# Kernel tuning notes

Hardware: AMD Instinct MI355X
Metric: run time of the kernel (lower is better)

Reference implementation:

```python
import jax, jax.numpy as jnp
import numpy as np
from jax import lax

WBITS = 2
ABITS = 2
STRIDES = (1, 1)
PADDING = 'SAME'


def _ste_quantize(x, k):
    # round(x * n) / n with straight-through gradient (identity)
    n = float(2 ** k - 1)
    q = jnp.round(x * n) / n
    return x + lax.stop_gradient(q - x)


def _quantize_weight(w, k):
    # DoReFa-style weight quantization: tanh, normalize to [0,1], quantize, map to [-1,1]
    t = jnp.tanh(w)
    t = t / jnp.max(jnp.abs(t)) * 0.5 + 0.5
    return 2.0 * _ste_quantize(t, k) - 1.0


def _quantize_act(x, k):
    return _ste_quantize(jnp.clip(x, 0.0, 1.0), k)


def setup_inputs() -> dict:
    key = jax.random.key(0)
    kx, kw = jax.random.split(key)
    x = jax.random.uniform(kx, (32, 56, 56, 256), dtype=jnp.float32)  # NHWC
    w = jax.random.normal(kw, (3, 3, 256, 256), dtype=jnp.float32) * 0.2  # HWIO
    # match init normalization: unit L2 norm per output channel over (h,w,cin)
    w = w / jnp.sqrt(1e-7 + jnp.sum(w * w, axis=(0, 1, 2), keepdims=True))
    return {'x': x, 'w': w}


def reference(x, w) -> jnp.ndarray:
    wq = _quantize_weight(w, WBITS)        # low-bit weights in [-1, 1]
    xq = _quantize_act(x, ABITS)           # low-bit activations in [0, 1]
    out = lax.conv_general_dilated(
        xq, wq,
        window_strides=STRIDES,
        padding=PADDING,
        dimension_numbers=('NHWC', 'HWIO', 'NHWC'),
    )
    return out
```

## Files before the change

kernel.cpp:

```cpp
#include <hip/hip_runtime.h>
#include <stdint.h>

#define GLOBAL_AS __attribute__((address_space(1)))
#define LDS_AS    __attribute__((address_space(3)))

typedef int   v4i  __attribute__((ext_vector_type(4)));
typedef int   v8i  __attribute__((ext_vector_type(8)));
typedef float v16f __attribute__((ext_vector_type(16)));

__device__ __forceinline__ void gload_lds16(const void* g, void* l) {
    __builtin_amdgcn_global_load_lds((GLOBAL_AS uint32_t*)g, (LDS_AS uint32_t*)l, 16, 0, 0);
}


__global__ void k_xq_wmax(const float* __restrict__ x, const float* __restrict__ w,
                          int8_t* __restrict__ xqp, unsigned* __restrict__ maxbits) {
    const int bid = blockIdx.x;
    if (bid < 48) {
        int t = bid * 256 + threadIdx.x;
        const float4* w4 = (const float4*)w;
        float m = 0.f;
        for (int i = t; i < 147456; i += 12288) {
            float4 v = w4[i];
            m = fmaxf(m, fmaxf(fmaxf(fabsf(tanhf(v.x)), fabsf(tanhf(v.y))),
                               fmaxf(fabsf(tanhf(v.z)), fabsf(tanhf(v.w)))));
        }
#pragma unroll
        for (int off = 32; off > 0; off >>= 1)
            m = fmaxf(m, __shfl_xor(m, off, 64));
        if ((threadIdx.x & 63) == 0) atomicMax(maxbits, __float_as_uint(m));
        return;
    }
    int t = (bid - 48) * 256 + threadIdx.x;
    int g  = t & 7;
    int p  = t >> 3;
    int xp = p % 58;
    int q  = p / 58;
    int yp = q % 58;
    int n  = q / 58;
    int4 r;
    if (yp == 0 || yp == 57 || xp == 0 || xp == 57) {
        r = make_int4(0, 0, 0, 0);
    } else {
        const float4* px = (const float4*)(x + (((long)((n * 56 + (yp - 1)) * 56 + (xp - 1))) << 8) + g * 32);
        int wds[4];
#pragma unroll
        for (int jj = 0; jj < 4; ++jj) {
            float4 v0 = px[jj * 2];
            float4 v1 = px[jj * 2 + 1];
            int q0 = (int)rintf(fminf(fmaxf(v0.x, 0.f), 1.f) * 3.f);
            int q1 = (int)rintf(fminf(fmaxf(v0.y, 0.f), 1.f) * 3.f);
            int q2 = (int)rintf(fminf(fmaxf(v0.z, 0.f), 1.f) * 3.f);
            int q3 = (int)rintf(fminf(fmaxf(v0.w, 0.f), 1.f) * 3.f);
            int q4 = (int)rintf(fminf(fmaxf(v1.x, 0.f), 1.f) * 3.f);
            int q5 = (int)rintf(fminf(fmaxf(v1.y, 0.f), 1.f) * 3.f);
            int q6 = (int)rintf(fminf(fmaxf(v1.z, 0.f), 1.f) * 3.f);
            int q7 = (int)rintf(fminf(fmaxf(v1.w, 0.f), 1.f) * 3.f);
            wds[jj] = ((0x5420 >> (q0 << 2)) & 0xF)        | (((0x5420 >> (q1 << 2)) & 0xF) << 4)
                    | (((0x5420 >> (q2 << 2)) & 0xF) << 8) | (((0x5420 >> (q3 << 2)) & 0xF) << 12)
                    | (((0x5420 >> (q4 << 2)) & 0xF) << 16)| (((0x5420 >> (q5 << 2)) & 0xF) << 20)
                    | (((0x5420 >> (q6 << 2)) & 0xF) << 24)| (((0x5420 >> (q7 << 2)) & 0xF) << 28);
        }
        r = make_int4(wds[0], wds[1], wds[2], wds[3]);
    }
    *(int4*)(xqp + ((long)t << 4)) = r;
}

__global__ void k_wq(const float* __restrict__ w, const unsigned* __restrict__ maxbits,
                     int8_t* __restrict__ wqt) {
    int t = blockIdx.x * 256 + threadIdx.x;
    int co = t & 255;
    int kblk = t >> 8;
    float inv = 0.5f / __uint_as_float(*maxbits);
    uint8_t b[16];
#pragma unroll
    for (int j = 0; j < 16; ++j) {
        float t0 = tanhf(w[(long)(kblk * 32 + 2 * j) * 256 + co]);
        float t1 = tanhf(w[(long)(kblk * 32 + 2 * j + 1) * 256 + co]);
        int q0 = (int)rintf((t0 * inv + 0.5f) * 3.0f);
        int q1 = (int)rintf((t1 * inv + 0.5f) * 3.0f);
        b[j] = (uint8_t)(((0x52AD >> (q0 << 2)) & 0xF) | (((0x52AD >> (q1 << 2)) & 0xF) << 4));
    }
    *(int4*)(wqt + (long)co * 1152 + kblk * 16) = *(int4*)b;
}

#define BM 128
#define BN 128

__global__ __launch_bounds__(256) void k_conv(const int8_t* __restrict__ xqp,
                                              const int8_t* __restrict__ wqt,
                                              float* __restrict__ out) {
    __shared__ int8_t sA[2][BM * 128];
    __shared__ int8_t sB[2][BN * 128];

    const int tid    = threadIdx.x;
    const int wv     = tid >> 6;
    const int lane   = tid & 63;
    const int orig   = blockIdx.x;
    const int work   = (orig & 7) * 196 + (orig >> 3);
    const int coBase = (work & 1) * BN;
    const int mBase  = (work >> 1) * BM;

    const int lr = lane >> 3;
    const int lp = lane & 7;
    const int8_t* aB[4];
    const int8_t* bB[4];
#pragma unroll
    for (int j = 0; j < 4; ++j) {
        int r = wv * 8 + j * 32 + lr;
        int g = lp ^ (r & 7);
        int m = mBase + r;
        int n = m / 3136;
        int rem = m - n * 3136;
        int y = rem / 56;
        int x = rem - y * 56;
        aB[j] = xqp + (((long)((n * 58 + y) * 58 + x)) << 7) + g * 16;
        bB[j] = wqt + (long)(coBase + r) * 1152 + g * 16;
    }

    v16f acc[2][2];
#pragma unroll
    for (int a = 0; a < 2; ++a)
#pragma unroll
        for (int b = 0; b < 2; ++b)
#pragma unroll
            for (int r = 0; r < 16; ++r) acc[a][b][r] = 0.f;

    const int wm  = (wv & 1) * 64;
    const int wn  = (wv >> 1) * 64;
    const int l31 = lane & 31;
    const int hi  = lane >> 5;

    const int rA0 = (wm + l31) * 128;       const int axr0 = ((wm + l31) & 7) << 4;
    const int rA1 = (wm + 32 + l31) * 128;  const int axr1 = ((wm + 32 + l31) & 7) << 4;
    const int rB0 = (wn + l31) * 128;       const int bxr0 = ((wn + l31) & 7) << 4;
    const int rB1 = (wn + 32 + l31) * 128;  const int bxr1 = ((wn + 32 + l31) & 7) << 4;

    auto issue = [&](int it, int b) {
        int ky  = it / 3;
        int kx  = it - ky * 3;
        int aOff = (ky * 58 + kx) << 7;
        int bOff = it << 7;
#pragma unroll
        for (int j = 0; j < 4; ++j) {
            gload_lds16(aB[j] + aOff, &sA[b][(wv * 8 + j * 32) * 128]);
            gload_lds16(bB[j] + bOff, &sB[b][(wv * 8 + j * 32) * 128]);
        }
    };

    const int SC = 0x7F7F7F7F;

    auto compute = [&](int b) {
        const int8_t* pA = sA[b];
        const int8_t* pB = sB[b];
        __builtin_amdgcn_s_setprio(1);
#pragma unroll
        for (int kk = 0; kk < 4; ++kk) {
            const int kc = (kk * 2 + hi) << 4;
            v4i a0 = *(const v4i*)(pA + rA0 + (kc ^ axr0));
            v4i a1 = *(const v4i*)(pA + rA1 + (kc ^ axr1));
            v4i b0 = *(const v4i*)(pB + rB0 + (kc ^ bxr0));
            v4i b1 = *(const v4i*)(pB + rB1 + (kc ^ bxr1));
            v8i A0 = {a0[0], a0[1], a0[2], a0[3], 0, 0, 0, 0};
            v8i A1 = {a1[0], a1[1], a1[2], a1[3], 0, 0, 0, 0};
            v8i B0 = {b0[0], b0[1], b0[2], b0[3], 0, 0, 0, 0};
            v8i B1 = {b1[0], b1[1], b1[2], b1[3], 0, 0, 0, 0};
            acc[0][0] = __builtin_amdgcn_mfma_scale_f32_32x32x64_f8f6f4(A0, B0, acc[0][0], 4, 4, 0, SC, 0, SC);
            acc[0][1] = __builtin_amdgcn_mfma_scale_f32_32x32x64_f8f6f4(A0, B1, acc[0][1], 4, 4, 0, SC, 0, SC);
            acc[1][0] = __builtin_amdgcn_mfma_scale_f32_32x32x64_f8f6f4(A1, B0, acc[1][0], 4, 4, 0, SC, 0, SC);
            acc[1][1] = __builtin_amdgcn_mfma_scale_f32_32x32x64_f8f6f4(A1, B1, acc[1][1], 4, 4, 0, SC, 0, SC);
        }
        __builtin_amdgcn_s_setprio(0);
    };

    issue(0, 0);
#pragma unroll 2
    for (int it = 0; it < 8; ++it) {
        issue(it + 1, (it + 1) & 1);
        asm volatile("s_waitcnt vmcnt(8)" ::: "memory");
        __builtin_amdgcn_s_barrier();
        asm volatile("" ::: "memory");
        compute(it & 1);
        asm volatile("" ::: "memory");
        __builtin_amdgcn_s_barrier();
        asm volatile("" ::: "memory");
    }
    asm volatile("s_waitcnt vmcnt(0)" ::: "memory");
    __builtin_amdgcn_s_barrier();
    asm volatile("" ::: "memory");
    compute(0);

    const float s = 1.0f / 9.0f;
#pragma unroll
    for (int mt = 0; mt < 2; ++mt) {
#pragma unroll
        for (int nt = 0; nt < 2; ++nt) {
            const int ocol = coBase + wn + nt * 32 + l31;
#pragma unroll
            for (int reg = 0; reg < 16; ++reg) {
                const int row = (reg & 3) + 8 * (reg >> 2) + 4 * hi;
                const long orow = mBase + wm + mt * 32 + row;
                out[orow * 256 + ocol] = acc[mt][nt][reg] * s;
            }
        }
    }
}

extern "C" void kernel_launch(void* const* d_in, const int* in_sizes, int n_in,
                              void* d_out, int out_size, void* d_ws, size_t ws_size,
                              hipStream_t stream) {
    const float* x = (const float*)d_in[0];
    const float* w = (const float*)d_in[1];
    float* out = (float*)d_out;

    unsigned* maxbits = (unsigned*)d_ws;
    int8_t* wqt = (int8_t*)d_ws + 4096;
    int8_t* xqp = (int8_t*)d_ws + 4096 + 294912;

    hipMemsetAsync(maxbits, 0, 4, stream);
    k_xq_wmax<<<48 + 3364, 256, 0, stream>>>(x, w, xqp, maxbits);
    k_wq<<<72, 256, 0, stream>>>(w, maxbits, wqt);
    k_conv<<<1568, 256, 0, stream>>>(xqp, wqt, out);
}
```

Before: 229.7 us.

## Stage halo pixel tile in LDS once and stream weights into registers

Each block now loads a single 256-pixel halo tile of padded, quantized activations into LDS once. All nine 3x3 taps are served from that tile by shifting the pixel offset, instead of reloading a 128-row A tile per tap. Weights are read directly from global memory into double-buffered registers, which removes the LDS B buffers and the per-iteration barriers. Tiles now follow image boundaries (25 tiles of 128 pixels per image), so some rows are computed and then masked at the store. Register pressure also rises from holding the B fragments.

```diff
diff --git a/kernel.cpp b/kernel.cpp
--- a/kernel.cpp
+++ b/kernel.cpp
@@ -84,113 +84,106 @@
     *(int4*)(wqt + (long)co * 1152 + kblk * 16) = *(int4*)b;
 }
 
-#define BM 128
-#define BN 128
-
-__global__ __launch_bounds__(256) void k_conv(const int8_t* __restrict__ xqp,
-                                              const int8_t* __restrict__ wqt,
-                                              float* __restrict__ out) {
-    __shared__ int8_t sA[2][BM * 128];
-    __shared__ int8_t sB[2][BN * 128];
-
-    const int tid    = threadIdx.x;
-    const int wv     = tid >> 6;
-    const int lane   = tid & 63;
-    const int orig   = blockIdx.x;
-    const int work   = (orig & 7) * 196 + (orig >> 3);
-    const int coBase = (work & 1) * BN;
-    const int mBase  = (work >> 1) * BM;
-
-    const int lr = lane >> 3;
-    const int lp = lane & 7;
-    const int8_t* aB[4];
-    const int8_t* bB[4];
-#pragma unroll
-    for (int j = 0; j < 4; ++j) {
-        int r = wv * 8 + j * 32 + lr;
-        int g = lp ^ (r & 7);
-        int m = mBase + r;
-        int n = m / 3136;
-        int rem = m - n * 3136;
-        int y = rem / 56;
-        int x = rem - y * 56;
-        aB[j] = xqp + (((long)((n * 58 + y) * 58 + x)) << 7) + g * 16;
-        bB[j] = wqt + (long)(coBase + r) * 1152 + g * 16;
-    }
-
-    v16f acc[2][2];
-#pragma unroll
-    for (int a = 0; a < 2; ++a)
-#pragma unroll
-        for (int b = 0; b < 2; ++b)
-#pragma unroll
-            for (int r = 0; r < 16; ++r) acc[a][b][r] = 0.f;
+__global__ __launch_bounds__(256, 3) void k_conv(const int8_t* __restrict__ xqp,
+                                                 const int8_t* __restrict__ wqt,
+                                                 float* __restrict__ out) {
+    __shared__ int8_t sX[256 * 128];
+
+    const int tid  = threadIdx.x;
+    const int wv   = tid >> 6;
+    const int lane = tid & 63;
+    const int orig = blockIdx.x;
+    const int work = (orig & 7) * 200 + (orig >> 3);
+    const int coBase = (work & 1) << 7;
+    const int wt   = work >> 1;
+    const int n    = wt / 25;
+    const int t    = wt - n * 25;
+
+    const int m0 = t * 128;
+    const int y0 = m0 / 56;
+    const int x0 = m0 - y0 * 56;
+    const long pixBase = ((long)(n * 58 + y0)) * 58 + x0;
+
+    {
+        const int lr = lane >> 3;
+        const int lp = lane & 7;
+#pragma unroll
+        for (int j = 0; j < 8; ++j) {
+            int p = wv * 8 + j * 32 + lr;
+            int g = lp ^ (p & 7);
+            long pg = pixBase + p;
+            if (pg > 107647) pg = 107647;
+            gload_lds16(xqp + (pg << 7) + g * 16, &sX[(wv * 8 + j * 32) * 128]);
+        }
+    }
 
     const int wm  = (wv & 1) * 64;
     const int wn  = (wv >> 1) * 64;
     const int l31 = lane & 31;
     const int hi  = lane >> 5;
-
-    const int rA0 = (wm + l31) * 128;       const int axr0 = ((wm + l31) & 7) << 4;
-    const int rA1 = (wm + 32 + l31) * 128;  const int axr1 = ((wm + 32 + l31) & 7) << 4;
-    const int rB0 = (wn + l31) * 128;       const int bxr0 = ((wn + l31) & 7) << 4;
-    const int rB1 = (wn + 32 + l31) * 128;  const int bxr1 = ((wn + 32 + l31) & 7) << 4;
-
-    auto issue = [&](int it, int b) {
-        int ky  = it / 3;
-        int kx  = it - ky * 3;
-        int aOff = (ky * 58 + kx) << 7;
-        int bOff = it << 7;
-#pragma unroll
-        for (int j = 0; j < 4; ++j) {
-            gload_lds16(aB[j] + aOff, &sA[b][(wv * 8 + j * 32) * 128]);
-            gload_lds16(bB[j] + bOff, &sB[b][(wv * 8 + j * 32) * 128]);
+    const int h16 = hi << 4;
+
+    const int8_t* pB0 = wqt + (long)(coBase + wn + l31) * 1152 + h16;
+    const int8_t* pB1 = pB0 + 32 * 1152;
+
+    int mL0 = m0 + wm + l31;      if (mL0 > 3135) mL0 = 3135;
+    int mL1 = m0 + wm + 32 + l31; if (mL1 > 3135) mL1 = 3135;
+    const int yR0 = mL0 / 56, xR0 = mL0 - yR0 * 56;
+    const int yR1 = mL1 / 56, xR1 = mL1 - yR1 * 56;
+    const int po0 = (yR0 - y0) * 58 + (xR0 - x0);
+    const int po1 = (yR1 - y0) * 58 + (xR1 - x0);
+
+    v16f acc[2][2];
+#pragma unroll
+    for (int a = 0; a < 2; ++a)
+#pragma unroll
+        for (int b = 0; b < 2; ++b)
+#pragma unroll
+            for (int r = 0; r < 16; ++r) acc[a][b][r] = 0.f;
+
+    v4i bR[2][2][4];
+    auto loadB = [&](int it, int s) {
+#pragma unroll
+        for (int kk = 0; kk < 4; ++kk) {
+            bR[s][0][kk] = *(const v4i*)(pB0 + it * 128 + kk * 32);
+            bR[s][1][kk] = *(const v4i*)(pB1 + it * 128 + kk * 32);
         }
     };
 
+    loadB(0, 0);
+    __syncthreads();
+
     const int SC = 0x7F7F7F7F;
-
-    auto compute = [&](int b) {
-        const int8_t* pA = sA[b];
-        const int8_t* pB = sB[b];
+#pragma unroll
+    for (int it = 0; it < 9; ++it) {
+        if (it < 8) loadB(it + 1, (it + 1) & 1);
+        const int tapoff = (it / 3) * 58 + (it % 3);
+        const int pL0 = po0 + tapoff;
+        const int pL1 = po1 + tapoff;
+        const int8_t* a0b = sX + pL0 * 128;
+        const int8_t* a1b = sX + pL1 * 128;
+        const int xx0 = (pL0 & 7) << 4;
+        const int xx1 = (pL1 & 7) << 4;
         __builtin_amdgcn_s_setprio(1);
 #pragma unroll
         for (int kk = 0; kk < 4; ++kk) {
-            const int kc = (kk * 2 + hi) << 4;
-            v4i a0 = *(const v4i*)(pA + rA0 + (kc ^ axr0));
-            v4i a1 = *(const v4i*)(pA + rA1 + (kc ^ axr1));
-            v4i b0 = *(const v4i*)(pB + rB0 + (kc ^ bxr0));
-            v4i b1 = *(const v4i*)(pB + rB1 + (kc ^ bxr1));
+            const int kc = kk * 32 + h16;
+            v4i a0 = *(const v4i*)(a0b + (kc ^ xx0));
+            v4i a1 = *(const v4i*)(a1b + (kc ^ xx1));
             v8i A0 = {a0[0], a0[1], a0[2], a0[3], 0, 0, 0, 0};
             v8i A1 = {a1[0], a1[1], a1[2], a1[3], 0, 0, 0, 0};
-            v8i B0 = {b0[0], b0[1], b0[2], b0[3], 0, 0, 0, 0};
-            v8i B1 = {b1[0], b1[1], b1[2], b1[3], 0, 0, 0, 0};
+            v8i B0 = {bR[it & 1][0][kk][0], bR[it & 1][0][kk][1], bR[it & 1][0][kk][2], bR[it & 1][0][kk][3], 0, 0, 0, 0};
+            v8i B1 = {bR[it & 1][1][kk][0], bR[it & 1][1][kk][1], bR[it & 1][1][kk][2], bR[it & 1][1][kk][3], 0, 0, 0, 0};
             acc[0][0] = __builtin_amdgcn_mfma_scale_f32_32x32x64_f8f6f4(A0, B0, acc[0][0], 4, 4, 0, SC, 0, SC);
             acc[0][1] = __builtin_amdgcn_mfma_scale_f32_32x32x64_f8f6f4(A0, B1, acc[0][1], 4, 4, 0, SC, 0, SC);
             acc[1][0] = __builtin_amdgcn_mfma_scale_f32_32x32x64_f8f6f4(A1, B0, acc[1][0], 4, 4, 0, SC, 0, SC);
             acc[1][1] = __builtin_amdgcn_mfma_scale_f32_32x32x64_f8f6f4(A1, B1, acc[1][1], 4, 4, 0, SC, 0, SC);
         }
         __builtin_amdgcn_s_setprio(0);
-    };
-
-    issue(0, 0);
-#pragma unroll 2
-    for (int it = 0; it < 8; ++it) {
-        issue(it + 1, (it + 1) & 1);
-        asm volatile("s_waitcnt vmcnt(8)" ::: "memory");
-        __builtin_amdgcn_s_barrier();
-        asm volatile("" ::: "memory");
-        compute(it & 1);
-        asm volatile("" ::: "memory");
-        __builtin_amdgcn_s_barrier();
-        asm volatile("" ::: "memory");
-    }
-    asm volatile("s_waitcnt vmcnt(0)" ::: "memory");
-    __builtin_amdgcn_s_barrier();
-    asm volatile("" ::: "memory");
-    compute(0);
+    }
 
     const float s = 1.0f / 9.0f;
+    const long outImg = (long)n * 3136;
 #pragma unroll
     for (int mt = 0; mt < 2; ++mt) {
 #pragma unroll
@@ -199,8 +192,9 @@
 #pragma unroll
             for (int reg = 0; reg < 16; ++reg) {
                 const int row = (reg & 3) + 8 * (reg >> 2) + 4 * hi;
-                const long orow = mBase + wm + mt * 32 + row;
-                out[orow * 256 + ocol] = acc[mt][nt][reg] * s;
+                const int rowLocal = m0 + wm + mt * 32 + row;
+                if (rowLocal < 3136)
+                    out[(outImg + rowLocal) * 256 + ocol] = acc[mt][nt][reg] * s;
             }
         }
     }
@@ -220,5 +214,5 @@
     hipMemsetAsync(maxbits, 0, 4, stream);
     k_xq_wmax<<<48 + 3364, 256, 0, stream>>>(x, w, xqp, maxbits);
     k_wq<<<72, 256, 0, stream>>>(w, maxbits, wqt);
-    k_conv<<<1568, 256, 0, stream>>>(xqp, wqt, out);
-}
+    k_conv<<<1600, 256, 0, stream>>>(xqp, wqt, out);
+}
```

After: 555.6 us. +141.9%, slower.
